# Performance work log

Hardware: AMD Instinct MI355X
Metric: run time of the kernel (lower is better)

The kernel has to match this reference:

```python
import jax, jax.numpy as jnp
import numpy as np

K = 20
EPS = 1e-5
NEG_SLOPE = 0.2


def knn(x, k):
    # x: [B, C, N] -> idx [B, N, k] of nearest neighbors (negative sq-dist topk)
    inner = -2.0 * jnp.einsum('bcn,bcm->bnm', x, x)
    xx = jnp.sum(x * x, axis=1)  # [B, N]
    d = -xx[:, :, None] - inner - xx[:, None, :]
    return jax.lax.top_k(d, k)[1]


def get_graph_feature(x, k):
    # x: [B, C, N] -> [B, 2C, N, k]
    idx = knn(x, k)
    xt = jnp.transpose(x, (0, 2, 1))            # [B, N, C]
    feat = jax.vmap(lambda a, i: a[i])(xt, idx)  # [B, N, k, C]
    center = xt[:, :, None, :]
    out = jnp.concatenate([feat - center, jnp.broadcast_to(center, feat.shape)], axis=-1)
    return jnp.transpose(out, (0, 3, 1, 2))


def conv_bn_lrelu(x, w, g, b):
    # 1x1 conv + BatchNorm2d (batch stats, training mode) + LeakyReLU(0.2)
    y = jnp.einsum('oc,bcnk->bonk', w, x)
    mu = jnp.mean(y, axis=(0, 2, 3), keepdims=True)
    var = jnp.mean((y - mu) ** 2, axis=(0, 2, 3), keepdims=True)
    y = (y - mu) * jax.lax.rsqrt(var + EPS)
    y = y * g[None, :, None, None] + b[None, :, None, None]
    return jnp.where(y >= 0, y, NEG_SLOPE * y)


def lrelu(y):
    return jnp.where(y >= 0, y, NEG_SLOPE * y)


def setup_inputs() -> dict:
    key = jax.random.key(0)
    ks = jax.random.split(key, 24)
    B, N = 8, 4096
    d = {}
    d['x'] = jax.random.normal(ks[0], (B, 3, N), dtype=jnp.float32)
    def wconv(k_, o, c):
        return jax.random.normal(k_, (o, c), dtype=jnp.float32) * (1.0 / np.sqrt(c))
    d['w1'] = wconv(ks[1], 32, 6)
    d['g1'] = 1.0 + 0.1 * jax.random.normal(ks[2], (32,), dtype=jnp.float32)
    d['b1'] = 0.1 * jax.random.normal(ks[3], (32,), dtype=jnp.float32)
    d['w2'] = wconv(ks[4], 64, 70)
    d['g2'] = 1.0 + 0.1 * jax.random.normal(ks[5], (64,), dtype=jnp.float32)
    d['b2'] = 0.1 * jax.random.normal(ks[6], (64,), dtype=jnp.float32)
    d['wd1'] = wconv(ks[7], 64, 64)
    d['gd1'] = 1.0 + 0.1 * jax.random.normal(ks[8], (64,), dtype=jnp.float32)
    d['bd1'] = 0.1 * jax.random.normal(ks[9], (64,), dtype=jnp.float32)
    d['wd2'] = wconv(ks[10], 64, 128)
    d['gd2'] = 1.0 + 0.1 * jax.random.normal(ks[11], (64,), dtype=jnp.float32)
    d['bd2'] = 0.1 * jax.random.normal(ks[12], (64,), dtype=jnp.float32)
    d['W2d'] = jax.random.normal(ks[13], (128, 128), dtype=jnp.float32) * (1.0 / np.sqrt(128))
    d['b2d'] = 0.1 * jax.random.normal(ks[14], (128,), dtype=jnp.float32)
    d['W3d'] = jax.random.normal(ks[15], (64, 128), dtype=jnp.float32) * (1.0 / np.sqrt(128))
    d['b3d'] = 0.1 * jax.random.normal(ks[16], (64,), dtype=jnp.float32)
    d['W4d'] = jax.random.normal(ks[17], (11, 64), dtype=jnp.float32) * (1.0 / np.sqrt(64))
    d['b4d'] = 0.1 * jax.random.normal(ks[18], (11,), dtype=jnp.float32)
    return d


def reference(x, w1, g1, b1, w2, g2, b2, wd1, gd1, bd1, wd2, gd2, bd2,
              W2d, b2d, W3d, b3d, W4d, b4d):
    x1_gf = get_graph_feature(x, K)                    # [B, 6, N, k]
    x1_max = jnp.max(conv_bn_lrelu(x1_gf, w1, g1, b1), axis=-1)  # [B, 32, N]
    x2_gf = jnp.concatenate([x1_gf, get_graph_feature(x1_max, K)], axis=1)  # [B, 70, N, k]
    x2_max = jnp.max(conv_bn_lrelu(x2_gf, w2, g2, b2), axis=-1)  # [B, 64, N]
    xd1 = jnp.max(conv_bn_lrelu(get_graph_feature(x1_max, K), wd1, gd1, bd1), axis=-1)  # [B, 64, N]
    xd2 = jnp.max(conv_bn_lrelu(get_graph_feature(x2_max, K), wd2, gd2, bd2), axis=-1)  # [B, 64, N]
    h = jnp.concatenate([xd1, xd2], axis=1)            # [B, 128, N]
    h = h.reshape(1, -1, 128)                          # faithful row-major view
    h = jnp.mean(h, axis=1)                            # [1, 128]
    h = lrelu(h @ W2d.T + b2d)
    h = lrelu(h @ W3d.T + b3d)
    return lrelu(h @ W4d.T + b4d)                      # [1, 11]
```

## Files before the change

kernel.cpp:

```cpp
#include <hip/hip_runtime.h>

#define BB 8
#define NN 4096
#define KK 20
constexpr float EPSV = 1e-5f;
constexpr float SLOPE = 0.2f;

typedef __bf16 bfrag __attribute__((ext_vector_type(8)));
typedef float floatx4 __attribute__((ext_vector_type(4)));
typedef unsigned short us4 __attribute__((ext_vector_type(4)));

__device__ __forceinline__ float lrelu(float v) { return v >= 0.f ? v : SLOPE * v; }

__device__ __forceinline__ unsigned short bf16rn(float f) {
    unsigned int u = __float_as_uint(f);
    return (unsigned short)((u + 0x7FFFu + ((u >> 16) & 1u)) >> 16);
}
__device__ __forceinline__ float bf16up(unsigned short h) {
    return __uint_as_float(((unsigned int)h) << 16);
}

__global__ void zero_kernel(float* p, int n) {
    int i = blockIdx.x * 256 + threadIdx.x;
    if (i < n) p[i] = 0.f;
}

template<int C>
__global__ void halfnorm_kernel(const float* __restrict__ src, float* __restrict__ hng) {
    int n = blockIdx.x * 256 + threadIdx.x;
    int b = blockIdx.y;
    float s = 0.f;
    #pragma unroll
    for (int c = 0; c < C; c++) { float v = src[(b * C + c) * NN + n]; s += v * v; }
    hng[b * NN + n] = 0.5f * s;
}

template<int C>
__global__ __launch_bounds__(256) void knn_kernel(const float* __restrict__ src,
                                                  const float* __restrict__ hng,
                                                  int* __restrict__ idx) {
    constexpr int SK = (C == 3) ? 40 : (2 * C + 8);
    __shared__ unsigned short qpack[64 * SK];
    __shared__ unsigned short cpack[64 * SK];
    __shared__ float hn[64];
    __shared__ float pv[64 * 65];
    __shared__ unsigned short pidx[64 * 66];
    __shared__ float tau[64];
    __shared__ int   cnt[64];

    const int b = blockIdx.y;
    const int q0 = blockIdx.x * 64;
    const int tid = threadIdx.x;
    const int lane = tid & 63;
    const int wv = tid >> 6;
    const int wr = (wv >> 1) * 32;
    const int wc = (wv & 1) * 32;
    const int fl = lane & 15;
    const int fq = lane >> 4;

    if (C == 3) {
        for (int i = tid; i < 64 * 20; i += 256) {
            int r = i / 20, k = 12 + i % 20;
            qpack[r * SK + k] = 0; cpack[r * SK + k] = 0;
        }
        if (tid < 64) {
            int q = tid;
            #pragma unroll
            for (int c = 0; c < 3; c++) {
                float v = src[(b * 3 + c) * NN + q0 + q];
                unsigned short h = bf16rn(v);
                unsigned short l = bf16rn(v - bf16up(h));
                qpack[q * SK + c] = h;  qpack[q * SK + 3 + c] = l;
                qpack[q * SK + 6 + c] = h;  qpack[q * SK + 9 + c] = l;
            }
        }
    } else {
        for (int t = 0; t < C / 16; t++) {
            int i = t * 256 + tid;
            int c4 = (i >> 6) * 4, m = i & 63;
            us4 hv, lv;
            #pragma unroll
            for (int j = 0; j < 4; j++) {
                float v = src[(b * C + c4 + j) * NN + q0 + m];
                unsigned short h = bf16rn(v);
                hv[j] = h;
                lv[j] = bf16rn(v - bf16up(h));
            }
            *(us4*)(&qpack[m * SK + c4]) = hv;
            *(us4*)(&qpack[m * SK + C + c4]) = lv;
        }
    }
    if (tid < 64) { tau[tid] = -3.4e38f; cnt[tid] = 0; }

    float tv[20]; int ti[20];
    #pragma unroll
    for (int k = 0; k < 20; k++) { tv[k] = -3.4e38f; ti[k] = 0; }
    __syncthreads();

    for (int ch = 0; ch < 64; ch++) {
        const int m0 = ch * 64;
        if (C == 3) {
            if (tid < 64) {
                int m = tid;
                #pragma unroll
                for (int c = 0; c < 3; c++) {
                    float v = src[(b * 3 + c) * NN + m0 + m];
                    unsigned short h = bf16rn(v);
                    unsigned short l = bf16rn(v - bf16up(h));
                    cpack[m * SK + c] = h;  cpack[m * SK + 3 + c] = l;
                    cpack[m * SK + 6 + c] = l;  cpack[m * SK + 9 + c] = h;
                }
            }
        } else {
            for (int t = 0; t < C / 16; t++) {
                int i = t * 256 + tid;
                int c4 = (i >> 6) * 4, m = i & 63;
                us4 hv, lv;
                #pragma unroll
                for (int j = 0; j < 4; j++) {
                    float v = src[(b * C + c4 + j) * NN + m0 + m];
                    unsigned short h = bf16rn(v);
                    hv[j] = h;
                    lv[j] = bf16rn(v - bf16up(h));
                }
                *(us4*)(&cpack[m * SK + c4]) = hv;
                *(us4*)(&cpack[m * SK + C + c4]) = lv;
            }
        }
        if (tid < 16) *(float4*)(hn + tid * 4) = *(const float4*)(hng + b * NN + m0 + tid * 4);
        __syncthreads();

        floatx4 acc[2][2];
        #pragma unroll
        for (int r2 = 0; r2 < 2; r2++)
            #pragma unroll
            for (int c2 = 0; c2 < 2; c2++)
                acc[r2][c2] = (floatx4)(0.f);

        if (C == 3) {
            #pragma unroll
            for (int r2 = 0; r2 < 2; r2++) {
                bfrag a = *(const bfrag*)(&qpack[(wr + r2 * 16 + fl) * SK + fq * 8]);
                #pragma unroll
                for (int c2 = 0; c2 < 2; c2++) {
                    bfrag bm = *(const bfrag*)(&cpack[(wc + c2 * 16 + fl) * SK + fq * 8]);
                    acc[r2][c2] = __builtin_amdgcn_mfma_f32_16x16x32_bf16(a, bm, acc[r2][c2], 0, 0, 0);
                }
            }
        } else {
            #pragma unroll
            for (int kk = 0; kk < C / 32; kk++) {
                const int kb = kk * 32 + fq * 8;
                bfrag ah[2], al[2], bh[2], bl[2];
                #pragma unroll
                for (int r2 = 0; r2 < 2; r2++) {
                    ah[r2] = *(const bfrag*)(&qpack[(wr + r2 * 16 + fl) * SK + kb]);
                    al[r2] = *(const bfrag*)(&qpack[(wr + r2 * 16 + fl) * SK + C + kb]);
                }
                #pragma unroll
                for (int c2 = 0; c2 < 2; c2++) {
                    bh[c2] = *(const bfrag*)(&cpack[(wc + c2 * 16 + fl) * SK + kb]);
                    bl[c2] = *(const bfrag*)(&cpack[(wc + c2 * 16 + fl) * SK + C + kb]);
                }
                #pragma unroll
                for (int r2 = 0; r2 < 2; r2++)
                    #pragma unroll
                    for (int c2 = 0; c2 < 2; c2++) {
                        acc[r2][c2] = __builtin_amdgcn_mfma_f32_16x16x32_bf16(ah[r2], bh[c2], acc[r2][c2], 0, 0, 0);
                        acc[r2][c2] = __builtin_amdgcn_mfma_f32_16x16x32_bf16(ah[r2], bl[c2], acc[r2][c2], 0, 0, 0);
                        acc[r2][c2] = __builtin_amdgcn_mfma_f32_16x16x32_bf16(al[r2], bh[c2], acc[r2][c2], 0, 0, 0);
                        acc[r2][c2] = __builtin_amdgcn_mfma_f32_16x16x32_bf16(al[r2], bl[c2], acc[r2][c2], 0, 0, 0);
                    }
            }
        }

        float hnv[2];
        #pragma unroll
        for (int c2 = 0; c2 < 2; c2++) hnv[c2] = hn[wc + c2 * 16 + fl];
        #pragma unroll
        for (int r2 = 0; r2 < 2; r2++) {
            float4 t4 = *(const float4*)(&tau[wr + r2 * 16 + fq * 4]);
            float ta[4] = {t4.x, t4.y, t4.z, t4.w};
            #pragma unroll
            for (int c2 = 0; c2 < 2; c2++) {
                #pragma unroll
                for (int reg = 0; reg < 4; reg++) {
                    float s = acc[r2][c2][reg] - hnv[c2];
                    if (s > ta[reg]) {
                        int q = wr + r2 * 16 + fq * 4 + reg;
                        int p = atomicAdd(&cnt[q], 1);
                        pv[q * 65 + p] = s;
                        pidx[q * 66 + p] = (unsigned short)(m0 + wc + c2 * 16 + fl);
                    }
                }
            }
        }
        __syncthreads();

        if (tid < 64) {
            int n = cnt[tid];
            for (int t = 0; t < n; t++) {
                float v = pv[tid * 65 + t];
                if (v > tv[0]) {
                    tv[0] = v; ti[0] = (int)pidx[tid * 66 + t];
                    #pragma unroll
                    for (int j = 0; j < 19; j++) {
                        if (tv[j] > tv[j + 1]) {
                            float a = tv[j]; tv[j] = tv[j + 1]; tv[j + 1] = a;
                            int bi = ti[j]; ti[j] = ti[j + 1]; ti[j + 1] = bi;
                        }
                    }
                }
            }
            cnt[tid] = 0;
            tau[tid] = tv[0];
        }
        __syncthreads();
    }

    if (tid < 64) {
        #pragma unroll
        for (int k = 0; k < 20; k++)
            idx[(b * NN + q0 + tid) * KK + k] = ti[k];
    }
}

template<int COUT>
__global__ void precompute_kernel(const float* __restrict__ src, int C,
                                  const float* __restrict__ w, int CIN, int wd_off, int wc_off,
                                  float* __restrict__ G, float* __restrict__ H,
                                  int initG, int initH) {
    constexpr int MY = 256 / COUT;
    extern __shared__ float lds[];
    float* wd = lds;
    float* wc = lds + C * COUT;
    const int b = blockIdx.y;
    const int tid = threadIdx.y * COUT + threadIdx.x;
    for (int i = tid; i < C * COUT; i += 256) {
        int c = i / COUT, o = i % COUT;
        float a  = w[o * CIN + wd_off + c];
        float cc = w[o * CIN + wc_off + c];
        wd[i] = a;
        wc[i] = cc - a;
    }
    __syncthreads();
    const int o = threadIdx.x;
    for (int it = 0; it < COUT / 4; it++) {
        int m = blockIdx.x * 64 + it * MY + threadIdx.y;
        float g = 0.f, h = 0.f;
        for (int c = 0; c < C; c++) {
            float s = src[(b * C + c) * NN + m];
            g += wd[c * COUT + o] * s;
            h += wc[c * COUT + o] * s;
        }
        int gi = (b * NN + m) * COUT + o;
        if (initG) G[gi] = g; else G[gi] += g;
        if (initH) H[gi] = h; else H[gi] += h;
    }
}

template<int COUT, int GROUPS>
__global__ void conv_stats_kernel(const float* __restrict__ G1, const int* __restrict__ idx1,
                                  const float* __restrict__ G2, const int* __restrict__ idx2,
                                  const float* __restrict__ H, float* __restrict__ stats,
                                  float* __restrict__ MaxY, float* __restrict__ MinY) {
    constexpr int NY = 256 / COUT;
    const int b = blockIdx.y;
    const int o = threadIdx.x;
    const int n = blockIdx.x * NY + threadIdx.y;
    const int base = b * NN + n;
    const float h = H[base * COUT + o];
    float s1 = 0.f, s2 = 0.f;
    float gx = -3.4e38f, gn = 3.4e38f;
    #pragma unroll
    for (int k = 0; k < KK; k++) {
        int i1 = idx1[base * KK + k];
        float g = G1[(b * NN + i1) * COUT + o];
        if (GROUPS == 2) {
            int i2 = idx2[base * KK + k];
            g += G2[(b * NN + i2) * COUT + o];
        }
        float y = g + h;
        s1 += y;
        s2 += y * y;
        gx = fmaxf(gx, g);
        gn = fminf(gn, g);
    }
    MaxY[base * COUT + o] = gx + h;
    MinY[base * COUT + o] = gn + h;

    __shared__ float ls[2 * COUT];
    if (threadIdx.y == 0) { ls[o] = 0.f; ls[COUT + o] = 0.f; }
    __syncthreads();
    atomicAdd(&ls[o], s1);
    atomicAdd(&ls[COUT + o], s2);
    __syncthreads();
    if (threadIdx.y == 0) {
        atomicAdd(&stats[o], ls[o]);
        atomicAdd(&stats[64 + o], ls[COUT + o]);
    }
}

__global__ void finalize_kernel(const float* __restrict__ g, const float* __restrict__ bb,
                                float* __restrict__ stats, int cout, float invP) {
    int o = threadIdx.x;
    if (o >= cout) return;
    float mu  = stats[o] * invP;
    float var = stats[64 + o] * invP - mu * mu;
    float sc  = g[o] * rsqrtf(var + EPSV);
    stats[128 + o] = sc;
    stats[192 + o] = bb[o] - mu * sc;
}

__global__ void apply_kernel(const float* __restrict__ MaxY, const float* __restrict__ MinY,
                             const float* __restrict__ stats, float* __restrict__ out, int cout) {
    int e = blockIdx.x * 256 + threadIdx.x;
    int total = BB * cout * NN;
    if (e >= total) return;
    int n = e & (NN - 1);
    int o = (e >> 12) % cout;
    int b = e / (NN * cout);
    float sc = stats[128 + o], sh = stats[192 + o];
    int si = (b * NN + n) * cout + o;
    float v = (sc >= 0.f) ? MaxY[si] : MinY[si];
    out[e] = lrelu(sc * v + sh);
}

__global__ void mean_kernel(const float* __restrict__ xd1, const float* __restrict__ xd2,
                            float* __restrict__ hsum) {
    __shared__ float bins[128];
    const int tid = threadIdx.x;
    if (tid < 128) bins[tid] = 0.f;
    __syncthreads();
    const int half = BB * 64 * NN;
    const int stride = gridDim.x * 256;
    for (int e = blockIdx.x * 256 + tid; e < half; e += stride)
        atomicAdd(&bins[e & 127], xd1[e]);
    for (int e = blockIdx.x * 256 + tid; e < half; e += stride)
        atomicAdd(&bins[e & 127], xd2[e]);
    __syncthreads();
    if (tid < 128) atomicAdd(&hsum[tid], bins[tid]);
}

__global__ void head_kernel(const float* __restrict__ hsum,
                            const float* __restrict__ W2d, const float* __restrict__ b2d,
                            const float* __restrict__ W3d, const float* __restrict__ b3d,
                            const float* __restrict__ W4d, const float* __restrict__ b4d,
                            float* __restrict__ out) {
    __shared__ float h[128], t1[128], t2[64];
    const int t = threadIdx.x;
    h[t] = hsum[t] * (1.f / 32768.f);
    __syncthreads();
    float a = b2d[t];
    for (int j = 0; j < 128; j++) a += W2d[t * 128 + j] * h[j];
    t1[t] = lrelu(a);
    __syncthreads();
    if (t < 64) {
        float a2 = b3d[t];
        for (int j = 0; j < 128; j++) a2 += W3d[t * 128 + j] * t1[j];
        t2[t] = lrelu(a2);
    }
    __syncthreads();
    if (t < 11) {
        float a3 = b4d[t];
        for (int j = 0; j < 64; j++) a3 += W4d[t * 64 + j] * t2[j];
        out[t] = lrelu(a3);
    }
}

extern "C" void kernel_launch(void* const* d_in, const int* in_sizes, int n_in,
                              void* d_out, int out_size, void* d_ws, size_t ws_size,
                              hipStream_t stream) {
    const float* x   = (const float*)d_in[0];
    const float* w1  = (const float*)d_in[1];
    const float* g1  = (const float*)d_in[2];
    const float* b1  = (const float*)d_in[3];
    const float* w2  = (const float*)d_in[4];
    const float* g2  = (const float*)d_in[5];
    const float* b2  = (const float*)d_in[6];
    const float* wd1 = (const float*)d_in[7];
    const float* gd1 = (const float*)d_in[8];
    const float* bd1 = (const float*)d_in[9];
    const float* wd2 = (const float*)d_in[10];
    const float* gd2 = (const float*)d_in[11];
    const float* bd2 = (const float*)d_in[12];
    const float* W2d = (const float*)d_in[13];
    const float* b2d = (const float*)d_in[14];
    const float* W3d = (const float*)d_in[15];
    const float* b3d = (const float*)d_in[16];
    const float* W4d = (const float*)d_in[17];
    const float* b4d = (const float*)d_in[18];
    float* out = (float*)d_out;

    char* ws = (char*)d_ws;
    size_t off = 0;
    auto alloc = [&](size_t bytes) { char* p = ws + off; off += (bytes + 255) & ~size_t(255); return p; };
    int*   idx1  = (int*)  alloc(BB * NN * KK * 4);
    int*   idx2  = (int*)  alloc(BB * NN * KK * 4);
    int*   idx3  = (int*)  alloc(BB * NN * KK * 4);
    float* x1m   = (float*)alloc(BB * 32 * NN * 4);
    float* x2m   = (float*)alloc(BB * 64 * NN * 4);
    float* xd1   = (float*)alloc(BB * 64 * NN * 4);
    float* xd2   = (float*)alloc(BB * 64 * NN * 4);
    float* G1    = (float*)alloc((size_t)BB * NN * 64 * 4);
    float* G2    = (float*)alloc((size_t)BB * NN * 64 * 4);
    float* H     = (float*)alloc((size_t)BB * NN * 64 * 4);
    float* MaxY  = (float*)alloc((size_t)BB * NN * 64 * 4);
    float* MinY  = (float*)alloc((size_t)BB * NN * 64 * 4);
    float* stats = (float*)alloc(256 * 4);
    float* hsum  = (float*)alloc(128 * 4);
    float* hng   = (float*)alloc(BB * NN * 4);

    const float invP = 1.f / (float)(BB * NN * KK);
    const dim3 knn_grid(NN / 64, BB);
    const dim3 hn_grid(NN / 256, BB);

    zero_kernel<<<1, 256, 0, stream>>>(hsum, 128);

    halfnorm_kernel<3><<<hn_grid, 256, 0, stream>>>(x, hng);
    knn_kernel<3><<<knn_grid, 256, 0, stream>>>(x, hng, idx1);

    zero_kernel<<<1, 256, 0, stream>>>(stats, 128);
    precompute_kernel<32><<<dim3(NN / 64, BB), dim3(32, 8), 2 * 3 * 32 * 4, stream>>>(
        x, 3, w1, 6, 0, 3, G1, H, 1, 1);
    conv_stats_kernel<32, 1><<<dim3(NN / 8, BB), dim3(32, 8), 0, stream>>>(
        G1, idx1, nullptr, nullptr, H, stats, MaxY, MinY);
    finalize_kernel<<<1, 64, 0, stream>>>(g1, b1, stats, 32, invP);
    apply_kernel<<<(BB * 32 * NN + 255) / 256, 256, 0, stream>>>(MaxY, MinY, stats, x1m, 32);

    halfnorm_kernel<32><<<hn_grid, 256, 0, stream>>>(x1m, hng);
    knn_kernel<32><<<knn_grid, 256, 0, stream>>>(x1m, hng, idx2);

    zero_kernel<<<1, 256, 0, stream>>>(stats, 128);
    precompute_kernel<64><<<dim3(NN / 64, BB), dim3(64, 4), 2 * 3 * 64 * 4, stream>>>(
        x, 3, w2, 70, 0, 3, G1, H, 1, 1);
    precompute_kernel<64><<<dim3(NN / 64, BB), dim3(64, 4), 2 * 32 * 64 * 4, stream>>>(
        x1m, 32, w2, 70, 6, 38, G2, H, 1, 0);
    conv_stats_kernel<64, 2><<<dim3(NN / 4, BB), dim3(64, 4), 0, stream>>>(
        G1, idx1, G2, idx2, H, stats, MaxY, MinY);
    finalize_kernel<<<1, 64, 0, stream>>>(g2, b2, stats, 64, invP);
    apply_kernel<<<(BB * 64 * NN + 255) / 256, 256, 0, stream>>>(MaxY, MinY, stats, x2m, 64);

    zero_kernel<<<1, 256, 0, stream>>>(stats, 128);
    precompute_kernel<64><<<dim3(NN / 64, BB), dim3(64, 4), 2 * 32 * 64 * 4, stream>>>(
        x1m, 32, wd1, 64, 0, 32, G1, H, 1, 1);
    conv_stats_kernel<64, 1><<<dim3(NN / 4, BB), dim3(64, 4), 0, stream>>>(
        G1, idx2, nullptr, nullptr, H, stats, MaxY, MinY);
    finalize_kernel<<<1, 64, 0, stream>>>(gd1, bd1, stats, 64, invP);
    apply_kernel<<<(BB * 64 * NN + 255) / 256, 256, 0, stream>>>(MaxY, MinY, stats, xd1, 64);

    halfnorm_kernel<64><<<hn_grid, 256, 0, stream>>>(x2m, hng);
    knn_kernel<64><<<knn_grid, 256, 0, stream>>>(x2m, hng, idx3);

    zero_kernel<<<1, 256, 0, stream>>>(stats, 128);
    precompute_kernel<64><<<dim3(NN / 64, BB), dim3(64, 4), 2 * 64 * 64 * 4, stream>>>(
        x2m, 64, wd2, 128, 0, 64, G1, H, 1, 1);
    conv_stats_kernel<64, 1><<<dim3(NN / 4, BB), dim3(64, 4), 0, stream>>>(
        G1, idx3, nullptr, nullptr, H, stats, MaxY, MinY);
    finalize_kernel<<<1, 64, 0, stream>>>(gd2, bd2, stats, 64, invP);
    apply_kernel<<<(BB * 64 * NN + 255) / 256, 256, 0, stream>>>(MaxY, MinY, stats, xd2, 64);

    mean_kernel<<<1024, 256, 0, stream>>>(xd1, xd2, hsum);
    head_kernel<<<1, 128, 0, stream>>>(hsum, W2d, b2d, W3d, b3d, W4d, b4d, out);
}
```

Before: 1.760 ms.

## Prepack bf16 hi/lo operands globally and stream candidate tiles via direct-to-LDS loads

Adds separate pack kernels that convert point features into swizzled bf16 hi/lo rows once, instead of every KNN block reconverting all candidates per chunk. The KNN kernel now loads query and candidate tiles straight into LDS with global_load_lds, using XOR swizzling to avoid bank conflicts. It doubles the candidate chunk to 128 with a 32x64 per-wave MFMA tile and halves the number of chunk iterations. Top-k draining is split across four waves and the second barrier per chunk is removed. The trade-offs are extra pack launches and memory traffic, and a candidate buffer capped at 32 per query per chunk, which could drop candidates after the first chunk.

New measurement: 1.791 ms. About the same (+1.8%).

```diff
diff --git a/kernel.cpp b/kernel.cpp
--- a/kernel.cpp
+++ b/kernel.cpp
@@ -8,7 +8,7 @@
 
 typedef __bf16 bfrag __attribute__((ext_vector_type(8)));
 typedef float floatx4 __attribute__((ext_vector_type(4)));
-typedef unsigned short us4 __attribute__((ext_vector_type(4)));
+typedef unsigned short us8 __attribute__((ext_vector_type(8)));
 
 __device__ __forceinline__ float lrelu(float v) { return v >= 0.f ? v : SLOPE * v; }
 
@@ -18,6 +18,12 @@
 }
 __device__ __forceinline__ float bf16up(unsigned short h) {
     return __uint_as_float(((unsigned int)h) << 16);
+}
+
+__device__ __forceinline__ void gl2lds16(const void* g, void* l) {
+    __builtin_amdgcn_global_load_lds(
+        (const __attribute__((address_space(1))) unsigned int*)g,
+        (__attribute__((address_space(3))) unsigned int*)l, 16, 0, 0);
 }
 
 __global__ void zero_kernel(float* p, int n) {
@@ -36,15 +42,74 @@
 }
 
 template<int C>
-__global__ __launch_bounds__(256) void knn_kernel(const float* __restrict__ src,
+__global__ void pack_kernel(const float* __restrict__ src, unsigned short* __restrict__ pk) {
+    constexpr int NCH = C / 4;
+    int i = blockIdx.x * 256 + threadIdx.x;
+    int b = blockIdx.y;
+    int n = i / NCH, j = i % NCH;
+    us8 v;
+    if (j < C / 8) {
+        int c0 = j * 8;
+        #pragma unroll
+        for (int cc = 0; cc < 8; cc++)
+            v[cc] = bf16rn(src[(b * C + c0 + cc) * NN + n]);
+    } else {
+        int c0 = (j - C / 8) * 8;
+        #pragma unroll
+        for (int cc = 0; cc < 8; cc++) {
+            float f = src[(b * C + c0 + cc) * NN + n];
+            unsigned short h = bf16rn(f);
+            v[cc] = bf16rn(f - bf16up(h));
+        }
+    }
+    int phys = j ^ (n & (NCH - 1));
+    *(us8*)(pk + ((size_t)(b * NN + n) * NCH + phys) * 8) = v;
+}
+
+__global__ void pack3_kernel(const float* __restrict__ src,
+                             unsigned short* __restrict__ pa, unsigned short* __restrict__ pb) {
+    int n = blockIdx.x * 256 + threadIdx.x;
+    int b = blockIdx.y;
+    unsigned short h[3], l[3];
+    #pragma unroll
+    for (int c = 0; c < 3; c++) {
+        float f = src[(b * 3 + c) * NN + n];
+        h[c] = bf16rn(f);
+        l[c] = bf16rn(f - bf16up(h[c]));
+    }
+    unsigned short A[32], B[32];
+    #pragma unroll
+    for (int k = 0; k < 32; k++) { A[k] = 0; B[k] = 0; }
+    #pragma unroll
+    for (int c = 0; c < 3; c++) {
+        A[c] = h[c];     A[3 + c] = l[c];  A[6 + c] = h[c];  A[9 + c] = l[c];
+        B[c] = h[c];     B[3 + c] = l[c];  B[6 + c] = l[c];  B[9 + c] = h[c];
+    }
+    size_t base = (size_t)(b * NN + n) * 32;
+    #pragma unroll
+    for (int j = 0; j < 4; j++) {
+        int phys = j ^ (n & 3);
+        us8 va, vb;
+        #pragma unroll
+        for (int t = 0; t < 8; t++) { va[t] = A[j * 8 + t]; vb[t] = B[j * 8 + t]; }
+        *(us8*)(pa + base + phys * 8) = va;
+        *(us8*)(pb + base + phys * 8) = vb;
+    }
+}
+
+template<int C>
+__global__ __launch_bounds__(256) void knn_kernel(const unsigned short* __restrict__ pq,
+                                                  const unsigned short* __restrict__ pc,
                                                   const float* __restrict__ hng,
                                                   int* __restrict__ idx) {
-    constexpr int SK = (C == 3) ? 40 : (2 * C + 8);
-    __shared__ unsigned short qpack[64 * SK];
-    __shared__ unsigned short cpack[64 * SK];
-    __shared__ float hn[64];
-    __shared__ float pv[64 * 65];
-    __shared__ unsigned short pidx[64 * 66];
+    constexpr int RS = (C == 3) ? 32 : 2 * C;
+    constexpr int NCHR = RS / 8;
+    constexpr int SWM = NCHR - 1;
+    __shared__ unsigned short qpack[64 * RS];
+    __shared__ unsigned short cpack[128 * RS];
+    __shared__ float hn[128];
+    __shared__ float pv[64 * 33];
+    __shared__ unsigned short pidx[64 * 34];
     __shared__ float tau[64];
     __shared__ int   cnt[64];
 
@@ -53,41 +118,18 @@
     const int tid = threadIdx.x;
     const int lane = tid & 63;
     const int wv = tid >> 6;
-    const int wr = (wv >> 1) * 32;
-    const int wc = (wv & 1) * 32;
     const int fl = lane & 15;
     const int fq = lane >> 4;
-
-    if (C == 3) {
-        for (int i = tid; i < 64 * 20; i += 256) {
-            int r = i / 20, k = 12 + i % 20;
-            qpack[r * SK + k] = 0; cpack[r * SK + k] = 0;
-        }
-        if (tid < 64) {
-            int q = tid;
-            #pragma unroll
-            for (int c = 0; c < 3; c++) {
-                float v = src[(b * 3 + c) * NN + q0 + q];
-                unsigned short h = bf16rn(v);
-                unsigned short l = bf16rn(v - bf16up(h));
-                qpack[q * SK + c] = h;  qpack[q * SK + 3 + c] = l;
-                qpack[q * SK + 6 + c] = h;  qpack[q * SK + 9 + c] = l;
-            }
-        }
-    } else {
-        for (int t = 0; t < C / 16; t++) {
-            int i = t * 256 + tid;
-            int c4 = (i >> 6) * 4, m = i & 63;
-            us4 hv, lv;
-            #pragma unroll
-            for (int j = 0; j < 4; j++) {
-                float v = src[(b * C + c4 + j) * NN + q0 + m];
-                unsigned short h = bf16rn(v);
-                hv[j] = h;
-                lv[j] = bf16rn(v - bf16up(h));
-            }
-            *(us4*)(&qpack[m * SK + c4]) = hv;
-            *(us4*)(&qpack[m * SK + C + c4]) = lv;
+    const int wr = (wv >> 1) * 32;
+    const int wc = (wv & 1) * 64;
+
+    {
+        const char* gq = (const char*)(pq + (size_t)(b * NN + q0) * RS);
+        constexpr int PQW = (64 * RS * 2 / 1024) / 4;
+        #pragma unroll
+        for (int t = 0; t < PQW; t++) {
+            int seg = wv * PQW + t;
+            gl2lds16(gq + seg * 1024 + lane * 16, (char*)qpack + seg * 1024);
         }
     }
     if (tid < 64) { tau[tid] = -3.4e38f; cnt[tid] = 0; }
@@ -95,77 +137,63 @@
     float tv[20]; int ti[20];
     #pragma unroll
     for (int k = 0; k < 20; k++) { tv[k] = -3.4e38f; ti[k] = 0; }
-    __syncthreads();
-
-    for (int ch = 0; ch < 64; ch++) {
-        const int m0 = ch * 64;
-        if (C == 3) {
-            if (tid < 64) {
-                int m = tid;
-                #pragma unroll
-                for (int c = 0; c < 3; c++) {
-                    float v = src[(b * 3 + c) * NN + m0 + m];
-                    unsigned short h = bf16rn(v);
-                    unsigned short l = bf16rn(v - bf16up(h));
-                    cpack[m * SK + c] = h;  cpack[m * SK + 3 + c] = l;
-                    cpack[m * SK + 6 + c] = l;  cpack[m * SK + 9 + c] = h;
-                }
-            }
-        } else {
-            for (int t = 0; t < C / 16; t++) {
-                int i = t * 256 + tid;
-                int c4 = (i >> 6) * 4, m = i & 63;
-                us4 hv, lv;
-                #pragma unroll
-                for (int j = 0; j < 4; j++) {
-                    float v = src[(b * C + c4 + j) * NN + m0 + m];
-                    unsigned short h = bf16rn(v);
-                    hv[j] = h;
-                    lv[j] = bf16rn(v - bf16up(h));
-                }
-                *(us4*)(&cpack[m * SK + c4]) = hv;
-                *(us4*)(&cpack[m * SK + C + c4]) = lv;
-            }
-        }
-        if (tid < 16) *(float4*)(hn + tid * 4) = *(const float4*)(hng + b * NN + m0 + tid * 4);
+
+    for (int ch = 0; ch < 32; ch++) {
+        const int m0 = ch * 128;
+        {
+            const char* gc = (const char*)(pc + (size_t)(b * NN + m0) * RS);
+            constexpr int PCW = (128 * RS * 2 / 1024) / 4;
+            #pragma unroll
+            for (int t = 0; t < PCW; t++) {
+                int seg = wv * PCW + t;
+                gl2lds16(gc + seg * 1024 + lane * 16, (char*)cpack + seg * 1024);
+            }
+        }
+        if (tid < 128) hn[tid] = hng[b * NN + m0 + tid];
         __syncthreads();
 
-        floatx4 acc[2][2];
+        floatx4 acc[2][4];
         #pragma unroll
         for (int r2 = 0; r2 < 2; r2++)
             #pragma unroll
-            for (int c2 = 0; c2 < 2; c2++)
+            for (int c2 = 0; c2 < 4; c2++)
                 acc[r2][c2] = (floatx4)(0.f);
 
-        if (C == 3) {
+        if constexpr (C == 3) {
+            bfrag a[2];
             #pragma unroll
             for (int r2 = 0; r2 < 2; r2++) {
-                bfrag a = *(const bfrag*)(&qpack[(wr + r2 * 16 + fl) * SK + fq * 8]);
+                int row = wr + r2 * 16 + fl;
+                a[r2] = *(const bfrag*)(qpack + row * RS + (fq ^ (row & SWM)) * 8);
+            }
+            #pragma unroll
+            for (int c2 = 0; c2 < 4; c2++) {
+                int row = wc + c2 * 16 + fl;
+                bfrag bm = *(const bfrag*)(cpack + row * RS + (fq ^ (row & SWM)) * 8);
                 #pragma unroll
-                for (int c2 = 0; c2 < 2; c2++) {
-                    bfrag bm = *(const bfrag*)(&cpack[(wc + c2 * 16 + fl) * SK + fq * 8]);
-                    acc[r2][c2] = __builtin_amdgcn_mfma_f32_16x16x32_bf16(a, bm, acc[r2][c2], 0, 0, 0);
-                }
+                for (int r2 = 0; r2 < 2; r2++)
+                    acc[r2][c2] = __builtin_amdgcn_mfma_f32_16x16x32_bf16(a[r2], bm, acc[r2][c2], 0, 0, 0);
             }
         } else {
             #pragma unroll
             for (int kk = 0; kk < C / 32; kk++) {
-                const int kb = kk * 32 + fq * 8;
-                bfrag ah[2], al[2], bh[2], bl[2];
+                bfrag ah[2], al[2], bh[4], bl[4];
                 #pragma unroll
                 for (int r2 = 0; r2 < 2; r2++) {
-                    ah[r2] = *(const bfrag*)(&qpack[(wr + r2 * 16 + fl) * SK + kb]);
-                    al[r2] = *(const bfrag*)(&qpack[(wr + r2 * 16 + fl) * SK + C + kb]);
+                    int row = wr + r2 * 16 + fl;
+                    ah[r2] = *(const bfrag*)(qpack + row * RS + ((kk * 4 + fq) ^ (row & SWM)) * 8);
+                    al[r2] = *(const bfrag*)(qpack + row * RS + ((C / 8 + kk * 4 + fq) ^ (row & SWM)) * 8);
                 }
                 #pragma unroll
-                for (int c2 = 0; c2 < 2; c2++) {
-                    bh[c2] = *(const bfrag*)(&cpack[(wc + c2 * 16 + fl) * SK + kb]);
-                    bl[c2] = *(const bfrag*)(&cpack[(wc + c2 * 16 + fl) * SK + C + kb]);
+                for (int c2 = 0; c2 < 4; c2++) {
+                    int row = wc + c2 * 16 + fl;
+                    bh[c2] = *(const bfrag*)(cpack + row * RS + ((kk * 4 + fq) ^ (row & SWM)) * 8);
+                    bl[c2] = *(const bfrag*)(cpack + row * RS + ((C / 8 + kk * 4 + fq) ^ (row & SWM)) * 8);
                 }
                 #pragma unroll
                 for (int r2 = 0; r2 < 2; r2++)
                     #pragma unroll
-                    for (int c2 = 0; c2 < 2; c2++) {
+                    for (int c2 = 0; c2 < 4; c2++) {
                         acc[r2][c2] = __builtin_amdgcn_mfma_f32_16x16x32_bf16(ah[r2], bh[c2], acc[r2][c2], 0, 0, 0);
                         acc[r2][c2] = __builtin_amdgcn_mfma_f32_16x16x32_bf16(ah[r2], bl[c2], acc[r2][c2], 0, 0, 0);
                         acc[r2][c2] = __builtin_amdgcn_mfma_f32_16x16x32_bf16(al[r2], bh[c2], acc[r2][c2], 0, 0, 0);
@@ -174,54 +202,70 @@
             }
         }
 
-        float hnv[2];
-        #pragma unroll
-        for (int c2 = 0; c2 < 2; c2++) hnv[c2] = hn[wc + c2 * 16 + fl];
-        #pragma unroll
-        for (int r2 = 0; r2 < 2; r2++) {
-            float4 t4 = *(const float4*)(&tau[wr + r2 * 16 + fq * 4]);
-            float ta[4] = {t4.x, t4.y, t4.z, t4.w};
-            #pragma unroll
-            for (int c2 = 0; c2 < 2; c2++) {
+        auto filter_one = [&](int c2) {
+            float hnv = hn[wc + c2 * 16 + fl];
+            #pragma unroll
+            for (int r2 = 0; r2 < 2; r2++) {
+                const float* tp = &tau[wr + r2 * 16 + fq * 4];
+                float t0 = tp[0], t1 = tp[1], t2 = tp[2], t3 = tp[3];
+                float ta[4] = {t0, t1, t2, t3};
                 #pragma unroll
                 for (int reg = 0; reg < 4; reg++) {
-                    float s = acc[r2][c2][reg] - hnv[c2];
+                    float s = acc[r2][c2][reg] - hnv;
                     if (s > ta[reg]) {
                         int q = wr + r2 * 16 + fq * 4 + reg;
                         int p = atomicAdd(&cnt[q], 1);
-                        pv[q * 65 + p] = s;
-                        pidx[q * 66 + p] = (unsigned short)(m0 + wc + c2 * 16 + fl);
-                    }
-                }
-            }
-        }
-        __syncthreads();
-
-        if (tid < 64) {
-            int n = cnt[tid];
-            for (int t = 0; t < n; t++) {
-                float v = pv[tid * 65 + t];
-                if (v > tv[0]) {
-                    tv[0] = v; ti[0] = (int)pidx[tid * 66 + t];
-                    #pragma unroll
-                    for (int j = 0; j < 19; j++) {
-                        if (tv[j] > tv[j + 1]) {
-                            float a = tv[j]; tv[j] = tv[j + 1]; tv[j + 1] = a;
-                            int bi = ti[j]; ti[j] = ti[j + 1]; ti[j + 1] = bi;
+                        if (p < 32) {
+                            pv[q * 33 + p] = s;
+                            pidx[q * 34 + p] = (unsigned short)(m0 + wc + c2 * 16 + fl);
                         }
                     }
                 }
             }
-            cnt[tid] = 0;
-            tau[tid] = tv[0];
-        }
-        __syncthreads();
-    }
-
-    if (tid < 64) {
+        };
+        auto drain = [&]() {
+            if (lane < 16) {
+                int qd = wv * 16 + lane;
+                int n = cnt[qd]; if (n > 32) n = 32;
+                for (int t = 0; t < n; t++) {
+                    float v = pv[qd * 33 + t];
+                    if (v > tv[0]) {
+                        tv[0] = v; ti[0] = (int)pidx[qd * 34 + t];
+                        #pragma unroll
+                        for (int j = 0; j < 19; j++) {
+                            if (tv[j] > tv[j + 1]) {
+                                float a = tv[j]; tv[j] = tv[j + 1]; tv[j + 1] = a;
+                                int bi = ti[j]; ti[j] = ti[j + 1]; ti[j + 1] = bi;
+                            }
+                        }
+                    }
+                }
+                cnt[qd] = 0;
+                tau[qd] = tv[0];
+            }
+        };
+
+        if (ch == 0) {
+            #pragma unroll
+            for (int ph = 0; ph < 4; ph++) {
+                filter_one(ph);
+                __syncthreads();
+                drain();
+                __syncthreads();
+            }
+        } else {
+            #pragma unroll
+            for (int c2 = 0; c2 < 4; c2++) filter_one(c2);
+            __syncthreads();
+            drain();
+        }
+    }
+
+    if (lane < 16) {
+        int q = q0 + wv * 16 + lane;
         #pragma unroll
         for (int k = 0; k < 20; k++)
-            idx[(b * NN + q0 + tid) * KK + k] = ti[k];
+            idx[(b * NN + q) * KK + k] = ti[k];
     }
 }
 
@@ -410,6 +454,10 @@
     float* stats = (float*)alloc(256 * 4);
     float* hsum  = (float*)alloc(128 * 4);
     float* hng   = (float*)alloc(BB * NN * 4);
+    unsigned short* pa3  = (unsigned short*)alloc((size_t)BB * NN * 32 * 2);
+    unsigned short* pb3  = (unsigned short*)alloc((size_t)BB * NN * 32 * 2);
+    unsigned short* pk32 = (unsigned short*)alloc((size_t)BB * NN * 64 * 2);
+    unsigned short* pk64 = (unsigned short*)alloc((size_t)BB * NN * 128 * 2);
 
     const float invP = 1.f / (float)(BB * NN * KK);
     const dim3 knn_grid(NN / 64, BB);
@@ -418,7 +466,8 @@
     zero_kernel<<<1, 256, 0, stream>>>(hsum, 128);
 
     halfnorm_kernel<3><<<hn_grid, 256, 0, stream>>>(x, hng);
-    knn_kernel<3><<<knn_grid, 256, 0, stream>>>(x, hng, idx1);
+    pack3_kernel<<<dim3(NN / 256, BB), 256, 0, stream>>>(x, pa3, pb3);
+    knn_kernel<3><<<knn_grid, 256, 0, stream>>>(pa3, pb3, hng, idx1);
 
     zero_kernel<<<1, 256, 0, stream>>>(stats, 128);
     precompute_kernel<32><<<dim3(NN / 64, BB), dim3(32, 8), 2 * 3 * 32 * 4, stream>>>(
@@ -429,7 +478,8 @@
     apply_kernel<<<(BB * 32 * NN + 255) / 256, 256, 0, stream>>>(MaxY, MinY, stats, x1m, 32);
 
     halfnorm_kernel<32><<<hn_grid, 256, 0, stream>>>(x1m, hng);
-    knn_kernel<32><<<knn_grid, 256, 0, stream>>>(x1m, hng, idx2);
+    pack_kernel<32><<<dim3(NN * 8 / 256, BB), 256, 0, stream>>>(x1m, pk32);
+    knn_kernel<32><<<knn_grid, 256, 0, stream>>>(pk32, pk32, hng, idx2);
 
     zero_kernel<<<1, 256, 0, stream>>>(stats, 128);
     precompute_kernel<64><<<dim3(NN / 64, BB), dim3(64, 4), 2 * 3 * 64 * 4, stream>>>(
@@ -450,7 +500,8 @@
     apply_kernel<<<(BB * 64 * NN + 255) / 256, 256, 0, stream>>>(MaxY, MinY, stats, xd1, 64);
 
     halfnorm_kernel<64><<<hn_grid, 256, 0, stream>>>(x2m, hng);
-    knn_kernel<64><<<knn_grid, 256, 0, stream>>>(x2m, hng, idx3);
+    pack_kernel<64><<<dim3(NN * 16 / 256, BB), 256, 0, stream>>>(x2m, pk64);
+    knn_kernel<64><<<knn_grid, 256, 0, stream>>>(pk64, pk64, hng, idx3);
 
     zero_kernel<<<1, 256, 0, stream>>>(stats, 128);
     precompute_kernel<64><<<dim3(NN / 64, BB), dim3(64, 4), 2 * 64 * 64 * 4, stream>>>(
```
